# Performance work log

Hardware: AMD Instinct MI355X
Metric: run time of the kernel (lower is better)

## Reference

```python
import jax, jax.numpy as jnp
import numpy as np

B, FIN, FOUT, FH2, NMIX, LAT, H, W = 16, 256, 256, 256, 8, 512, 64, 64


def _xavier(key, shape):
    # xavier_normal_ over last-two-ish dims; simple fan-based scale
    fan_in = int(np.prod(shape[1:]))
    fan_out = shape[0]
    s = (2.0 / (fan_in + fan_out)) ** 0.5
    return jax.random.normal(key, shape, jnp.float32) * s


def setup_inputs() -> dict:
    key = jax.random.key(0)
    ks = jax.random.split(key, 12)
    return {
        "x": jax.random.normal(ks[0], (B, FIN, H, W), jnp.float32),
        "lat": jax.random.normal(ks[1], (B, LAT), jnp.float32),
        # mixture kernel banks [n_mix, out_ch, in_ch] (kernel_size=1 squeezed)
        "k_in_mix": _xavier(ks[2], (NMIX, FH2, FIN)),
        "k_mid_mix": _xavier(ks[3], (NMIX, FH2, 2 * FH2)),
        "k_out_mix": _xavier(ks[4], (NMIX, FOUT, 2 * FH2)),
        "k_short_mix": _xavier(ks[5], (NMIX, FOUT, FIN)),
        # mixture bias banks [n_mix, ch]
        "b_in_mix": _xavier(ks[6], (NMIX, FH2)),
        "b_mid_mix": _xavier(ks[7], (NMIX, FH2)),
        "b_out_mix": _xavier(ks[8], (NMIX, FOUT)),
        "b_short_mix": _xavier(ks[9], (NMIX, FOUT)),
        # dyna_mix = nn.Linear(lat_size, n_mix) (lat_factor=0 path)
        "w_dyna": _xavier(ks[10], (NMIX, LAT)),
        "b_dyna": jnp.zeros((NMIX,), jnp.float32),
    }


def _complex_wave(h):
    # doubles channel dim: concat(sin, cos) along channels (per sample)
    return jnp.concatenate([jnp.sin(h), jnp.cos(h)], axis=1)


def reference(x, lat, k_in_mix, k_mid_mix, k_out_mix, k_short_mix,
              b_in_mix, b_mid_mix, b_out_mix, b_short_mix, w_dyna, b_dyna):
    # mixing coefficients per sample: [B, n_mix]
    mix = lat @ w_dyna.T + b_dyna
    # per-sample 1x1 conv kernels via mixture reduction: [B, out, in]
    k_in = jnp.einsum('bm,moi->boi', mix, k_in_mix)
    k_mid = jnp.einsum('bm,moi->boi', mix, k_mid_mix)
    k_out = jnp.einsum('bm,moi->boi', mix, k_out_mix)
    k_short = jnp.einsum('bm,moi->boi', mix, k_short_mix)
    # per-sample biases: [B, ch, 1, 1]
    b_in = (mix @ b_in_mix)[:, :, None, None]
    b_mid = (mix @ b_mid_mix)[:, :, None, None]
    b_out = (mix @ b_out_mix)[:, :, None, None]
    b_short = (mix @ b_short_mix)[:, :, None, None]
    # grouped conv with groups = batch (kernel_size=1) == per-sample matmul
    short = jnp.einsum('boi,bihw->bohw', k_short, x) + b_short
    h = jnp.einsum('boi,bihw->bohw', k_in, x) + b_in            # [B, FH2, H, W]
    h = _complex_wave(h)                                        # [B, 2*FH2, H, W]
    h = jnp.einsum('boi,bihw->bohw', k_mid, h) + b_mid
    h = _complex_wave(h)
    out = jnp.einsum('boi,bihw->bohw', k_out, h) + b_out + short
    return out
```

## Files before the change

### kernel.cpp

```cpp
#include <hip/hip_runtime.h>
#include <stdint.h>

#define B_    16
#define FIN   256
#define FOUT  256
#define FH2   256
#define NMIX  8
#define LAT   512
#define HW    4096
#define MT    64

typedef short bf16x8 __attribute__((ext_vector_type(8)));
typedef float f32x4  __attribute__((ext_vector_type(4)));

#define WS_MIX    0
#define WS_BIAS   1024
#define WS_WIN    131072
#define WS_WMID   2228224
#define WS_WOUT   6422528
#define WS_WSHORT 10616832

__device__ __forceinline__ uint16_t f2bf(float f) {
  uint32_t u = __builtin_bit_cast(uint32_t, f);
  u += 0x7fffu + ((u >> 16) & 1u);
  return (uint16_t)(u >> 16);
}
__device__ __forceinline__ uint32_t pack2(float lo, float hi) {
  return (uint32_t)f2bf(lo) | ((uint32_t)f2bf(hi) << 16);
}

#define MFMA(a, b, c) __builtin_amdgcn_mfma_f32_16x16x32_bf16(a, b, c, 0, 0, 0)

__global__ void k_mix_bias(const float* __restrict__ lat,
                           const float* __restrict__ w_dyna,
                           const float* __restrict__ b_dyna,
                           const float* __restrict__ b_in_mix,
                           const float* __restrict__ b_mid_mix,
                           const float* __restrict__ b_out_mix,
                           const float* __restrict__ b_short_mix,
                           float* __restrict__ ws_mix,
                           float* __restrict__ ws_bias) {
  __shared__ float smix[NMIX];
  const int t = threadIdx.x;
  const int lane = t & 63, wv = t >> 6;
  const int b = blockIdx.x;
#pragma unroll
  for (int d2 = 0; d2 < 2; d2++) {
    int m = wv * 2 + d2;
    float s = 0.f;
#pragma unroll
    for (int j = 0; j < 8; j++)
      s += lat[b * LAT + j * 64 + lane] * w_dyna[m * LAT + j * 64 + lane];
#pragma unroll
    for (int off = 32; off; off >>= 1) s += __shfl_xor(s, off);
    if (lane == 0) {
      float v = s + b_dyna[m];
      ws_mix[b * NMIX + m] = v;
      smix[m] = v;
    }
  }
  __syncthreads();
  const float* banks[4] = {b_in_mix, b_mid_mix, b_out_mix, b_short_mix};
  for (int pos = t; pos < 1024; pos += 256) {
    int bank = pos >> 8, ch = pos & 255;
    const float* bp = banks[bank];
    float a = 0.f;
#pragma unroll
    for (int m = 0; m < NMIX; m++) a += smix[m] * bp[m * 256 + ch];
    ws_bias[(bank * B_ + b) * 256 + ch] = a;
  }
}

__global__ void k_weights(const float* __restrict__ k_in_mix,
                          const float* __restrict__ k_mid_mix,
                          const float* __restrict__ k_out_mix,
                          const float* __restrict__ k_short_mix,
                          const float* __restrict__ ws_mix,
                          uint16_t* __restrict__ w_in,
                          uint16_t* __restrict__ w_mid,
                          uint16_t* __restrict__ w_out,
                          uint16_t* __restrict__ w_short) {
  __shared__ float smix[B_ * NMIX];
  const int t = threadIdx.x;
  if (t < B_ * NMIX) smix[t] = ws_mix[t];
  __syncthreads();
  const int e8 = (blockIdx.x * 256 + t) * 8;
  const float* srcA;
  uint16_t* dst;
  int sstride, dstride;
  bool ileave;
  if (e8 < 65536) {
    int e = e8;
    int lane = (e >> 3) & 63, ots = (e >> 9) & 3, kt = (e >> 11) & 7, wv = e >> 14;
    int row = wv * 64 + ots * 16 + (lane & 15);
    int k0 = kt * 32 + (lane >> 4) * 8;
    srcA = k_in_mix + row * 256 + k0; sstride = 65536; ileave = false;
    dst = w_in + e;                   dstride = 65536;
  } else if (e8 < 196608) {
    int e = e8 - 65536;
    int lane = (e >> 3) & 63, ots = (e >> 9) & 3, kt = (e >> 11) & 15, wv = e >> 15;
    int row = wv * 64 + ots * 16 + (lane & 15);
    int kp0 = kt * 32 + (lane >> 4) * 8;
    srcA = k_mid_mix + row * 512 + (kp0 >> 1); sstride = 131072; ileave = true;
    dst = w_mid + e;                           dstride = 131072;
  } else if (e8 < 327680) {
    int e = e8 - 196608;
    int lane = (e >> 3) & 63, ots = (e >> 9) & 3, kt = (e >> 11) & 15, wv = e >> 15;
    int row = wv * 64 + ots * 16 + (lane & 15);
    int kp0 = kt * 32 + (lane >> 4) * 8;
    srcA = k_out_mix + row * 512 + (kp0 >> 1); sstride = 131072; ileave = true;
    dst = w_out + e;                           dstride = 131072;
  } else {
    int e = e8 - 327680;
    int lane = (e >> 3) & 63, ots = (e >> 9) & 3, kt = (e >> 11) & 7, wv = e >> 14;
    int row = wv * 64 + ots * 16 + (lane & 15);
    int k0 = kt * 32 + (lane >> 4) * 8;
    srcA = k_short_mix + row * 256 + k0; sstride = 65536; ileave = false;
    dst = w_short + e;                   dstride = 65536;
  }
  const int boff = ileave ? 256 : 4;
  float4 va[NMIX], vb[NMIX];
#pragma unroll
  for (int m = 0; m < NMIX; m++) {
    va[m] = *(const float4*)(srcA + m * sstride);
    vb[m] = *(const float4*)(srcA + m * sstride + boff);
  }
  for (int b = 0; b < B_; b++) {
    float4 ra = make_float4(0.f, 0.f, 0.f, 0.f), rb = ra;
#pragma unroll
    for (int m = 0; m < NMIX; m++) {
      const float s = smix[b * NMIX + m];
      ra.x += s * va[m].x; ra.y += s * va[m].y; ra.z += s * va[m].z; ra.w += s * va[m].w;
      rb.x += s * vb[m].x; rb.y += s * vb[m].y; rb.z += s * vb[m].z; rb.w += s * vb[m].w;
    }
    int4 pkt;
    if (ileave) {
      pkt = make_int4((int)pack2(ra.x, rb.x), (int)pack2(ra.y, rb.y),
                      (int)pack2(ra.z, rb.z), (int)pack2(ra.w, rb.w));
    } else {
      pkt = make_int4((int)pack2(ra.x, ra.y), (int)pack2(ra.z, ra.w),
                      (int)pack2(rb.x, rb.y), (int)pack2(rb.z, rb.w));
    }
    *(int4*)(dst + (size_t)b * dstride) = pkt;
  }
}

__launch_bounds__(256, 2)
__global__ void k_main(const float* __restrict__ x,
                       const float* __restrict__ ws_bias,
                       const uint16_t* __restrict__ w_in,
                       const uint16_t* __restrict__ w_mid,
                       const uint16_t* __restrict__ w_out,
                       const uint16_t* __restrict__ w_short,
                       float* __restrict__ out) {
  __shared__ int4 smem4[73728 / 16];
  char* lds = (char*)smem4;
  char* Xc = lds;
  char* H1 = lds + 8192;

  const int t = threadIdx.x;
  const int lane = t & 63;
  const int wv = t >> 6;
  const int q = lane >> 4;
  const int n = lane & 15;
  const int b = blockIdx.x & 15;
  const int p0 = (blockIdx.x >> 4) * MT;

  const float* xb = x + (size_t)b * FIN * HW + p0;
  const int xpos = t & 63;
  const int xcg = wv;

  float xv[2][8];
#pragma unroll
  for (int e = 0; e < 8; e++)
    xv[0][e] = xb[(size_t)(0 * 32 + xcg * 8 + e) * HW + xpos];
#pragma unroll
  for (int e = 0; e < 8; e++)
    xv[1][e] = xb[(size_t)(1 * 32 + xcg * 8 + e) * HW + xpos];
  *(int4*)(Xc + xpos * 64 + ((xcg ^ (xpos & 3)) * 16)) =
      make_int4((int)pack2(xv[0][0], xv[0][1]), (int)pack2(xv[0][2], xv[0][3]),
                (int)pack2(xv[0][4], xv[0][5]), (int)pack2(xv[0][6], xv[0][7]));

  f32x4 acc_h[4][4], acc_s[4][4];
#pragma unroll
  for (int ots = 0; ots < 4; ots++) {
    const int o = wv * 64 + ots * 16 + q * 4;
    const float4 vi = *(const float4*)&ws_bias[(0 * B_ + b) * 256 + o];
    const float4 vs = *(const float4*)&ws_bias[(3 * B_ + b) * 256 + o];
    f32x4 ah, asv;
    ah[0] = vi.x; ah[1] = vi.y; ah[2] = vi.z; ah[3] = vi.w;
    asv[0] = vs.x; asv[1] = vs.y; asv[2] = vs.z; asv[3] = vs.w;
#pragma unroll
    for (int pt = 0; pt < 4; pt++) { acc_h[ots][pt] = ah; acc_s[ots][pt] = asv; }
  }

  const uint16_t* Wi = w_in + (size_t)b * 65536 + wv * 16384 + lane * 8;
  const uint16_t* Ws = w_short + (size_t)b * 65536 + wv * 16384 + lane * 8;
  bf16x8 ai[2][4], asf[2][4];
#pragma unroll
  for (int ots = 0; ots < 4; ots++) {
    ai[0][ots] = *(const bf16x8*)(Wi + ots * 512);
    asf[0][ots] = *(const bf16x8*)(Ws + ots * 512);
  }
  __syncthreads();

#pragma unroll
  for (int kt = 0; kt < 8; kt++) {
    if (kt < 6) {
      const float* xs = xb + (size_t)((kt + 2) * 32 + xcg * 8) * HW + xpos;
#pragma unroll
      for (int e = 0; e < 8; e++) xv[kt & 1][e] = xs[(size_t)e * HW];
    }
    if (kt < 7) {
#pragma unroll
      for (int ots = 0; ots < 4; ots++) {
        ai[(kt + 1) & 1][ots] = *(const bf16x8*)(Wi + (kt + 1) * 2048 + ots * 512);
        asf[(kt + 1) & 1][ots] = *(const bf16x8*)(Ws + (kt + 1) * 2048 + ots * 512);
      }
    }
    const char* Xr = Xc + (kt & 1) * 4096;
    bf16x8 bf[4];
#pragma unroll
    for (int pt = 0; pt < 4; pt++) {
      const int p = pt * 16 + n;
      bf[pt] = *(const bf16x8*)(Xr + p * 64 + ((q ^ (p & 3)) * 16));
    }
    __builtin_amdgcn_s_setprio(1);
#pragma unroll
    for (int ots = 0; ots < 4; ots++) {
#pragma unroll
      for (int pt = 0; pt < 4; pt++) {
        acc_h[ots][pt] = MFMA(ai[kt & 1][ots], bf[pt], acc_h[ots][pt]);
        acc_s[ots][pt] = MFMA(asf[kt & 1][ots], bf[pt], acc_s[ots][pt]);
      }
    }
    __builtin_amdgcn_s_setprio(0);
    if (kt < 7) {
      const int s = (kt + 1) & 1;
      *(int4*)(Xc + s * 4096 + xpos * 64 + ((xcg ^ (xpos & 3)) * 16)) =
          make_int4((int)pack2(xv[s][0], xv[s][1]), (int)pack2(xv[s][2], xv[s][3]),
                    (int)pack2(xv[s][4], xv[s][5]), (int)pack2(xv[s][6], xv[s][7]));
      __syncthreads();
    }
  }

#pragma unroll
  for (int ots = 0; ots < 4; ots++) {
    const int ctile = (wv * 4 + ots) * 4 + q;
#pragma unroll
    for (int pt = 0; pt < 4; pt++) {
      const int p = pt * 16 + n;
      *(int4*)(H1 + p * 1024 + ((ctile ^ (p & 7)) * 16)) = make_int4(
          (int)pack2(__sinf(acc_h[ots][pt][0]), __cosf(acc_h[ots][pt][0])),
          (int)pack2(__sinf(acc_h[ots][pt][1]), __cosf(acc_h[ots][pt][1])),
          (int)pack2(__sinf(acc_h[ots][pt][2]), __cosf(acc_h[ots][pt][2])),
          (int)pack2(__sinf(acc_h[ots][pt][3]), __cosf(acc_h[ots][pt][3])));
    }
  }

  const uint16_t* Wm = w_mid + (size_t)b * 131072 + wv * 32768 + lane * 8;
  bf16x8 am[4][4];
#pragma unroll
  for (int ots = 0; ots < 4; ots++) {
    am[0][ots] = *(const bf16x8*)(Wm + 0 * 2048 + ots * 512);
    am[1][ots] = *(const bf16x8*)(Wm + 1 * 2048 + ots * 512);
    am[2][ots] = *(const bf16x8*)(Wm + 2 * 2048 + ots * 512);
  }
  f32x4 acc2[4][4];
#pragma unroll
  for (int ots = 0; ots < 4; ots++) {
    const int o = wv * 64 + ots * 16 + q * 4;
    const float4 v = *(const float4*)&ws_bias[(1 * B_ + b) * 256 + o];
    f32x4 a2;
    a2[0] = v.x; a2[1] = v.y; a2[2] = v.z; a2[3] = v.w;
#pragma unroll
    for (int pt = 0; pt < 4; pt++) acc2[ots][pt] = a2;
  }
  __syncthreads();

#pragma unroll
  for (int kt = 0; kt < 16; kt++) {
    if (kt < 13) {
#pragma unroll
      for (int ots = 0; ots < 4; ots++)
        am[(kt + 3) & 3][ots] = *(const bf16x8*)(Wm + (kt + 3) * 2048 + ots * 512);
    }
    bf16x8 bf[4];
#pragma unroll
    for (int pt = 0; pt < 4; pt++) {
      const int p = pt * 16 + n;
      bf[pt] = *(const bf16x8*)(H1 + p * 1024 + (((kt * 4 + q) ^ (p & 7)) * 16));
    }
    __builtin_amdgcn_s_setprio(1);
#pragma unroll
    for (int ots = 0; ots < 4; ots++)
#pragma unroll
      for (int pt = 0; pt < 4; pt++)
        acc2[ots][pt] = MFMA(am[kt & 3][ots], bf[pt], acc2[ots][pt]);
    __builtin_amdgcn_s_setprio(0);
  }
  __syncthreads();

#pragma unroll
  for (int ots = 0; ots < 4; ots++) {
    const int ctile = (wv * 4 + ots) * 4 + q;
#pragma unroll
    for (int pt = 0; pt < 4; pt++) {
      const int p = pt * 16 + n;
      *(int4*)(H1 + p * 1024 + ((ctile ^ (p & 7)) * 16)) = make_int4(
          (int)pack2(__sinf(acc2[ots][pt][0]), __cosf(acc2[ots][pt][0])),
          (int)pack2(__sinf(acc2[ots][pt][1]), __cosf(acc2[ots][pt][1])),
          (int)pack2(__sinf(acc2[ots][pt][2]), __cosf(acc2[ots][pt][2])),
          (int)pack2(__sinf(acc2[ots][pt][3]), __cosf(acc2[ots][pt][3])));
    }
  }

  const uint16_t* Wo = w_out + (size_t)b * 131072 + wv * 32768 + lane * 8;
  bf16x8 ao[4][4];
#pragma unroll
  for (int ots = 0; ots < 4; ots++) {
    ao[0][ots] = *(const bf16x8*)(Wo + 0 * 2048 + ots * 512);
    ao[1][ots] = *(const bf16x8*)(Wo + 1 * 2048 + ots * 512);
    ao[2][ots] = *(const bf16x8*)(Wo + 2 * 2048 + ots * 512);
  }
#pragma unroll
  for (int ots = 0; ots < 4; ots++) {
    const int o = wv * 64 + ots * 16 + q * 4;
    const float4 v = *(const float4*)&ws_bias[(2 * B_ + b) * 256 + o];
#pragma unroll
    for (int pt = 0; pt < 4; pt++) {
      acc_s[ots][pt][0] += v.x; acc_s[ots][pt][1] += v.y;
      acc_s[ots][pt][2] += v.z; acc_s[ots][pt][3] += v.w;
    }
  }
  __syncthreads();

#pragma unroll
  for (int kt = 0; kt < 16; kt++) {
    if (kt < 13) {
#pragma unroll
      for (int ots = 0; ots < 4; ots++)
        ao[(kt + 3) & 3][ots] = *(const bf16x8*)(Wo + (kt + 3) * 2048 + ots * 512);
    }
    bf16x8 bf[4];
#pragma unroll
    for (int pt = 0; pt < 4; pt++) {
      const int p = pt * 16 + n;
      bf[pt] = *(const bf16x8*)(H1 + p * 1024 + (((kt * 4 + q) ^ (p & 7)) * 16));
    }
    __builtin_amdgcn_s_setprio(1);
#pragma unroll
    for (int ots = 0; ots < 4; ots++)
#pragma unroll
      for (int pt = 0; pt < 4; pt++)
        acc_s[ots][pt] = MFMA(ao[kt & 3][ots], bf[pt], acc_s[ots][pt]);
    __builtin_amdgcn_s_setprio(0);
  }

  {
    float* ob = out + (size_t)b * FOUT * HW + p0;
#pragma unroll
    for (int ots = 0; ots < 4; ots++) {
#pragma unroll
      for (int pt = 0; pt < 4; pt++) {
#pragma unroll
        for (int r = 0; r < 4; r++) {
          const int o = wv * 64 + ots * 16 + q * 4 + r;
          ob[(size_t)o * HW + pt * 16 + n] = acc_s[ots][pt][r];
        }
      }
    }
  }
}

extern "C" void kernel_launch(void* const* d_in, const int* in_sizes, int n_in,
                              void* d_out, int out_size, void* d_ws, size_t ws_size,
                              hipStream_t stream) {
  const float* x           = (const float*)d_in[0];
  const float* lat         = (const float*)d_in[1];
  const float* k_in_mix    = (const float*)d_in[2];
  const float* k_mid_mix   = (const float*)d_in[3];
  const float* k_out_mix   = (const float*)d_in[4];
  const float* k_short_mix = (const float*)d_in[5];
  const float* b_in_mix    = (const float*)d_in[6];
  const float* b_mid_mix   = (const float*)d_in[7];
  const float* b_out_mix   = (const float*)d_in[8];
  const float* b_short_mix = (const float*)d_in[9];
  const float* w_dyna      = (const float*)d_in[10];
  const float* b_dyna      = (const float*)d_in[11];

  char* ws = (char*)d_ws;
  float*    ws_mix  = (float*)(ws + WS_MIX);
  float*    ws_bias = (float*)(ws + WS_BIAS);
  uint16_t* w_in    = (uint16_t*)(ws + WS_WIN);
  uint16_t* w_mid   = (uint16_t*)(ws + WS_WMID);
  uint16_t* w_out   = (uint16_t*)(ws + WS_WOUT);
  uint16_t* w_short = (uint16_t*)(ws + WS_WSHORT);
  float* out = (float*)d_out;

  hipLaunchKernelGGL(k_mix_bias, dim3(16), dim3(256), 0, stream,
                     lat, w_dyna, b_dyna, b_in_mix, b_mid_mix, b_out_mix,
                     b_short_mix, ws_mix, ws_bias);
  hipLaunchKernelGGL(k_weights, dim3(192), dim3(256), 0, stream,
                     k_in_mix, k_mid_mix, k_out_mix, k_short_mix, ws_mix,
                     w_in, w_mid, w_out, w_short);
  hipLaunchKernelGGL(k_main, dim3(1024), dim3(256), 0, stream,
                     x, ws_bias, w_in, w_mid, w_out, w_short, out);
}
```

Baseline: 201.7 us.

## Stage x in 64-channel chunks and double-buffer LDS B-fragments in GEMM2/3

The first GEMM now stages x into LDS in 64-channel chunks instead of 32. Each thread loads 16 channels per chunk, the swizzle moves to a 128-byte row, and LDS grows to 80KB. This halves the number of __syncthreads barriers in the input/shortcut stage. The mid and out GEMM loops also prefetch the next k-step's LDS B-fragments into a register double buffer so LDS latency overlaps the MFMAs. The cost is extra LDS and register pressure, which could hurt occupancy at 2 blocks per CU.

```diff
diff --git a/kernel.cpp b/kernel.cpp
--- a/kernel.cpp
+++ b/kernel.cpp
@@ -153,10 +153,10 @@
                        const uint16_t* __restrict__ w_out,
                        const uint16_t* __restrict__ w_short,
                        float* __restrict__ out) {
-  __shared__ int4 smem4[73728 / 16];
+  __shared__ int4 smem4[81920 / 16];
   char* lds = (char*)smem4;
   char* Xc = lds;
-  char* H1 = lds + 8192;
+  char* H1 = lds + 16384;
 
   const int t = threadIdx.x;
   const int lane = t & 63;
@@ -168,18 +168,22 @@
 
   const float* xb = x + (size_t)b * FIN * HW + p0;
   const int xpos = t & 63;
-  const int xcg = wv;
 
   float xv[2][8];
 #pragma unroll
-  for (int e = 0; e < 8; e++)
-    xv[0][e] = xb[(size_t)(0 * 32 + xcg * 8 + e) * HW + xpos];
-#pragma unroll
-  for (int e = 0; e < 8; e++)
-    xv[1][e] = xb[(size_t)(1 * 32 + xcg * 8 + e) * HW + xpos];
-  *(int4*)(Xc + xpos * 64 + ((xcg ^ (xpos & 3)) * 16)) =
-      make_int4((int)pack2(xv[0][0], xv[0][1]), (int)pack2(xv[0][2], xv[0][3]),
-                (int)pack2(xv[0][4], xv[0][5]), (int)pack2(xv[0][6], xv[0][7]));
+  for (int u = 0; u < 2; u++) {
+    const int cg = wv * 2 + u;
+#pragma unroll
+    for (int e = 0; e < 8; e++)
+      xv[u][e] = xb[(size_t)(cg * 8 + e) * HW + xpos];
+  }
+#pragma unroll
+  for (int u = 0; u < 2; u++) {
+    const int cg = wv * 2 + u;
+    *(int4*)(Xc + xpos * 128 + ((cg ^ (xpos & 7)) * 16)) =
+        make_int4((int)pack2(xv[u][0], xv[u][1]), (int)pack2(xv[u][2], xv[u][3]),
+                  (int)pack2(xv[u][4], xv[u][5]), (int)pack2(xv[u][6], xv[u][7]));
+  }
 
   f32x4 acc_h[4][4], acc_s[4][4];
 #pragma unroll
@@ -205,41 +209,52 @@
   __syncthreads();
 
 #pragma unroll
-  for (int kt = 0; kt < 8; kt++) {
-    if (kt < 6) {
-      const float* xs = xb + (size_t)((kt + 2) * 32 + xcg * 8) * HW + xpos;
-#pragma unroll
-      for (int e = 0; e < 8; e++) xv[kt & 1][e] = xs[(size_t)e * HW];
-    }
-    if (kt < 7) {
+  for (int c = 0; c < 4; c++) {
+    if (c < 3) {
+#pragma unroll
+      for (int u = 0; u < 2; u++) {
+        const int cg = wv * 2 + u;
+#pragma unroll
+        for (int e = 0; e < 8; e++)
+          xv[u][e] = xb[(size_t)((c + 1) * 64 + cg * 8 + e) * HW + xpos];
+      }
+    }
+    const char* Xr = Xc + (c & 1) * 8192;
+#pragma unroll
+    for (int lh = 0; lh < 2; lh++) {
+      const int kt = c * 2 + lh;
+      if (kt < 7) {
+#pragma unroll
+        for (int ots = 0; ots < 4; ots++) {
+          ai[(kt + 1) & 1][ots] = *(const bf16x8*)(Wi + (kt + 1) * 2048 + ots * 512);
+          asf[(kt + 1) & 1][ots] = *(const bf16x8*)(Ws + (kt + 1) * 2048 + ots * 512);
+        }
+      }
+      bf16x8 bf[4];
+#pragma unroll
+      for (int pt = 0; pt < 4; pt++) {
+        const int p = pt * 16 + n;
+        bf[pt] = *(const bf16x8*)(Xr + p * 128 + (((lh * 4 + q) ^ (p & 7)) * 16));
+      }
+      __builtin_amdgcn_s_setprio(1);
 #pragma unroll
       for (int ots = 0; ots < 4; ots++) {
-        ai[(kt + 1) & 1][ots] = *(const bf16x8*)(Wi + (kt + 1) * 2048 + ots * 512);
-        asf[(kt + 1) & 1][ots] = *(const bf16x8*)(Ws + (kt + 1) * 2048 + ots * 512);
-      }
-    }
-    const char* Xr = Xc + (kt & 1) * 4096;
-    bf16x8 bf[4];
-#pragma unroll
-    for (int pt = 0; pt < 4; pt++) {
-      const int p = pt * 16 + n;
-      bf[pt] = *(const bf16x8*)(Xr + p * 64 + ((q ^ (p & 3)) * 16));
-    }
-    __builtin_amdgcn_s_setprio(1);
-#pragma unroll
-    for (int ots = 0; ots < 4; ots++) {
-#pragma unroll
-      for (int pt = 0; pt < 4; pt++) {
-        acc_h[ots][pt] = MFMA(ai[kt & 1][ots], bf[pt], acc_h[ots][pt]);
-        acc_s[ots][pt] = MFMA(asf[kt & 1][ots], bf[pt], acc_s[ots][pt]);
-      }
-    }
-    __builtin_amdgcn_s_setprio(0);
-    if (kt < 7) {
-      const int s = (kt + 1) & 1;
-      *(int4*)(Xc + s * 4096 + xpos * 64 + ((xcg ^ (xpos & 3)) * 16)) =
-          make_int4((int)pack2(xv[s][0], xv[s][1]), (int)pack2(xv[s][2], xv[s][3]),
-                    (int)pack2(xv[s][4], xv[s][5]), (int)pack2(xv[s][6], xv[s][7]));
+#pragma unroll
+        for (int pt = 0; pt < 4; pt++) {
+          acc_h[ots][pt] = MFMA(ai[kt & 1][ots], bf[pt], acc_h[ots][pt]);
+          acc_s[ots][pt] = MFMA(asf[kt & 1][ots], bf[pt], acc_s[ots][pt]);
+        }
+      }
+      __builtin_amdgcn_s_setprio(0);
+    }
+    if (c < 3) {
+#pragma unroll
+      for (int u = 0; u < 2; u++) {
+        const int cg = wv * 2 + u;
+        *(int4*)(Xc + ((c + 1) & 1) * 8192 + xpos * 128 + ((cg ^ (xpos & 7)) * 16)) =
+            make_int4((int)pack2(xv[u][0], xv[u][1]), (int)pack2(xv[u][2], xv[u][3]),
+                      (int)pack2(xv[u][4], xv[u][5]), (int)pack2(xv[u][6], xv[u][7]));
+      }
       __syncthreads();
     }
   }
@@ -278,26 +293,36 @@
   }
   __syncthreads();
 
-#pragma unroll
-  for (int kt = 0; kt < 16; kt++) {
-    if (kt < 13) {
-#pragma unroll
-      for (int ots = 0; ots < 4; ots++)
-        am[(kt + 3) & 3][ots] = *(const bf16x8*)(Wm + (kt + 3) * 2048 + ots * 512);
-    }
-    bf16x8 bf[4];
+  {
+    bf16x8 bfB[2][4];
 #pragma unroll
     for (int pt = 0; pt < 4; pt++) {
       const int p = pt * 16 + n;
-      bf[pt] = *(const bf16x8*)(H1 + p * 1024 + (((kt * 4 + q) ^ (p & 7)) * 16));
-    }
-    __builtin_amdgcn_s_setprio(1);
-#pragma unroll
-    for (int ots = 0; ots < 4; ots++)
-#pragma unroll
-      for (int pt = 0; pt < 4; pt++)
-        acc2[ots][pt] = MFMA(am[kt & 3][ots], bf[pt], acc2[ots][pt]);
-    __builtin_amdgcn_s_setprio(0);
+      bfB[0][pt] = *(const bf16x8*)(H1 + p * 1024 + ((q ^ (p & 7)) * 16));
+    }
+#pragma unroll
+    for (int kt = 0; kt < 16; kt++) {
+      if (kt < 15) {
+#pragma unroll
+        for (int pt = 0; pt < 4; pt++) {
+          const int p = pt * 16 + n;
+          bfB[(kt + 1) & 1][pt] =
+              *(const bf16x8*)(H1 + p * 1024 + ((((kt + 1) * 4 + q) ^ (p & 7)) * 16));
+        }
+      }
+      if (kt < 13) {
+#pragma unroll
+        for (int ots = 0; ots < 4; ots++)
+          am[(kt + 3) & 3][ots] = *(const bf16x8*)(Wm + (kt + 3) * 2048 + ots * 512);
+      }
+      __builtin_amdgcn_s_setprio(1);
+#pragma unroll
+      for (int ots = 0; ots < 4; ots++)
+#pragma unroll
+        for (int pt = 0; pt < 4; pt++)
+          acc2[ots][pt] = MFMA(am[kt & 3][ots], bfB[kt & 1][pt], acc2[ots][pt]);
+      __builtin_amdgcn_s_setprio(0);
+    }
   }
   __syncthreads();
 
@@ -335,26 +360,36 @@
   }
   __syncthreads();
 
-#pragma unroll
-  for (int kt = 0; kt < 16; kt++) {
-    if (kt < 13) {
-#pragma unroll
-      for (int ots = 0; ots < 4; ots++)
-        ao[(kt + 3) & 3][ots] = *(const bf16x8*)(Wo + (kt + 3) * 2048 + ots * 512);
-    }
-    bf16x8 bf[4];
+  {
+    bf16x8 bfC[2][4];
 #pragma unroll
     for (int pt = 0; pt < 4; pt++) {
       const int p = pt * 16 + n;
-      bf[pt] = *(const bf16x8*)(H1 + p * 1024 + (((kt * 4 + q) ^ (p & 7)) * 16));
-    }
-    __builtin_amdgcn_s_setprio(1);
-#pragma unroll
-    for (int ots = 0; ots < 4; ots++)
-#pragma unroll
-      for (int pt = 0; pt < 4; pt++)
-        acc_s[ots][pt] = MFMA(ao[kt & 3][ots], bf[pt], acc_s[ots][pt]);
-    __builtin_amdgcn_s_setprio(0);
+      bfC[0][pt] = *(const bf16x8*)(H1 + p * 1024 + ((q ^ (p & 7)) * 16));
+    }
+#pragma unroll
+    for (int kt = 0; kt < 16; kt++) {
+      if (kt < 15) {
+#pragma unroll
+        for (int pt = 0; pt < 4; pt++) {
+          const int p = pt * 16 + n;
+          bfC[(kt + 1) & 1][pt] =
+              *(const bf16x8*)(H1 + p * 1024 + ((((kt + 1) * 4 + q) ^ (p & 7)) * 16));
+        }
+      }
+      if (kt < 13) {
+#pragma unroll
+        for (int ots = 0; ots < 4; ots++)
+          ao[(kt + 3) & 3][ots] = *(const bf16x8*)(Wo + (kt + 3) * 2048 + ots * 512);
+      }
+      __builtin_amdgcn_s_setprio(1);
+#pragma unroll
+      for (int ots = 0; ots < 4; ots++)
+#pragma unroll
+        for (int pt = 0; pt < 4; pt++)
+          acc_s[ots][pt] = MFMA(ao[kt & 3][ots], bfC[kt & 1][pt], acc_s[ots][pt]);
+      __builtin_amdgcn_s_setprio(0);
+    }
   }
 
   {
```

After: 212.8 us. +5.5%, slower.
